# Kernel optimization log

Measured on AMD Instinct MI355X. Metric: run time of the kernel, lower is better.

## Reference

```python
import jax, jax.numpy as jnp
import numpy as np

N = 512
NODE_IN = 64
NODE_OUT = 64
ED_IN = 32
ED_OUT = 32
STATE = 80  # must satisfy 2*NODE_IN + ED_IN == 2*STATE
SLOPE = 0.1
EPS = 1e-5


def setup_inputs() -> dict:
    key = jax.random.key(0)
    ks = jax.random.split(key, 10)
    def lin(k, out_f, in_f):
        return jax.random.normal(k, (out_f, in_f), jnp.float32) / np.sqrt(in_f).astype(np.float32)
    x = jax.random.normal(ks[0], (N, NODE_IN), jnp.float32)
    edge_attr = jax.random.normal(ks[1], (N * N, ED_IN), jnp.float32)
    mask = jax.random.randint(ks[2], (N * N, 1), 0, 2).astype(jnp.int32)
    return {
        "x": x,
        "edge_attr": edge_attr,
        "mask": mask,
        "W_nu": lin(ks[3], NODE_OUT, NODE_IN),
        "b_nu": jnp.zeros((NODE_OUT,), jnp.float32),
        "W_h2": lin(ks[4], STATE, 2 * STATE),
        "b_h2": jnp.zeros((STATE,), jnp.float32),
        "W_eo": lin(ks[5], ED_OUT, STATE),
        "b_eo": jnp.zeros((ED_OUT,), jnp.float32),
        "e_vec": jax.random.normal(ks[6], (2 * NODE_OUT + ED_OUT,), jnp.float32) * 0.1,
        "bn_n_w": jnp.ones((NODE_OUT,), jnp.float32),
        "bn_n_b": jnp.zeros((NODE_OUT,), jnp.float32),
        "bn_e_w": jnp.ones((ED_OUT,), jnp.float32),
        "bn_e_b": jnp.zeros((ED_OUT,), jnp.float32),
    }


def _lrelu(v):
    return jax.nn.leaky_relu(v, SLOPE)


def _bn(v, w, b):
    # BatchNorm1d, training-mode (batch stats, biased variance)
    mu = v.mean(axis=0)
    var = v.var(axis=0)
    return (v - mu) / jnp.sqrt(var + EPS) * w + b


def reference(x, edge_attr, mask, W_nu, b_nu, W_h2, b_h2, W_eo, b_eo, e_vec,
              bn_n_w, bn_n_b, bn_e_w, bn_e_b):
    n = x.shape[0]
    m = mask.astype(x.dtype)  # [N*N, 1]
    # triplet_e[i*N+j] = [x_i, edge_attr_{ij}, x_j]
    src = jnp.repeat(x, n, axis=0)          # [N*N, NODE_IN]
    dst = jnp.tile(x, (n, 1))               # [N*N, NODE_IN]
    triplet_e = jnp.concatenate([src, edge_attr, dst], axis=-1)  # [N*N, 2*STATE]
    # NOTE: ed_trans_layer / ed_hidden_1 outputs are dead code in the source.
    h = _lrelu(triplet_e @ W_h2.T + b_h2)                 # [N*N, STATE]
    new_edge_attr = _lrelu(h @ W_eo.T + b_eo)             # [N*N, ED_OUT]
    new_edge_attr = new_edge_attr * m
    xn = _lrelu(x @ W_nu.T + b_nu)                        # [N, NODE_OUT]
    triplet_n = jnp.concatenate(
        [jnp.repeat(xn, n, axis=0), new_edge_attr, jnp.tile(xn, (n, 1))], axis=-1
    ).reshape(n, n, 2 * NODE_OUT + ED_OUT)
    scores = _lrelu(jnp.einsum("ijd,d->ij", triplet_n, e_vec))  # [N, N]
    att = jax.nn.softmax(scores, axis=1)
    att = (att.reshape(n * n, 1) * m).reshape(n, n)
    # dropout disabled (deterministic / eval)
    new_x = att @ xn                                       # [N, NODE_OUT]
    new_x = _bn(new_x, bn_n_w, bn_n_b)
    new_edge_attr = _bn(new_edge_attr, bn_e_w, bn_e_b)
    return new_x, new_edge_attr
```

## Files before the change

### kernel.cpp

```cpp
#include <hip/hip_runtime.h>

#define SLOPE 0.1f
#define EPS 1e-5f

typedef __bf16 bf16x8 __attribute__((ext_vector_type(8)));
typedef unsigned short u16x8 __attribute__((ext_vector_type(8)));
typedef float f32x4 __attribute__((ext_vector_type(4)));
typedef unsigned u32x4 __attribute__((ext_vector_type(4)));

#define WS_ESC 0
#define WS_ESH 32
#define WS_A 64
#define WS_B 576
#define WS_XN 1088
#define WS_NEWX 33856
#define WS_P1B 66624
#define WS_SC 107584
#define WS_PART 369728
#define WSH_WB 804992
#define WSH_WB2 810112
#define WSH_WO 812672
#define WSH_XB 815744
#define WSH_NE 848512

__device__ __forceinline__ float lrelu(float v) { return v > 0.f ? v : SLOPE * v; }
__device__ __forceinline__ unsigned short f2bf(float f) {
  unsigned x = __float_as_uint(f);
  return (unsigned short)((x + 0x7fffu + ((x >> 16) & 1u)) >> 16);
}
__device__ __forceinline__ float bf2f(unsigned short u) {
  return __uint_as_float(((unsigned)u) << 16);
}

__global__ void __launch_bounds__(256) k1(const float* __restrict__ x,
                                          const float* __restrict__ W_nu,
                                          const float* __restrict__ b_nu,
                                          const float* __restrict__ W_h2,
                                          const float* __restrict__ b_h2,
                                          const float* __restrict__ W_eo,
                                          const float* __restrict__ ev,
                                          float* ws) {
  int blk = blockIdx.x;
  int tid = threadIdx.x;
  unsigned short* wsh = (unsigned short*)ws;
  if (blk < 128) {
    __shared__ float wlds[64 * 65];
#pragma unroll
    for (int it = 0; it < 16; it++) {
      int idx = it * 256 + tid;
      wlds[(idx >> 6) * 65 + (idx & 63)] = W_nu[idx];
    }
    int gid = blk * 256 + tid;
    wsh[WSH_XB + gid] = f2bf(x[gid]);
    if (gid < 64) ws[WS_PART + gid] = 0.f;
    if (gid < 5120) {
      int c = gid / 2560, r = gid - c * 2560;
      int t = r >> 9, l = (r >> 3) & 63, jj = r & 7;
      int n = t * 16 + (l & 15);
      int k = (l >> 4) * 8 + jj + c * 32;
      wsh[WSH_WB + gid] = f2bf(W_h2[n * 160 + 64 + k]);
    } else if (gid < 7680) {
      int idx = gid - 5120;
      int t = idx >> 9, l = (idx >> 3) & 63, jj = idx & 7;
      int n = t * 16 + (l & 15);
      int k = (l >> 4) * 8 + jj;
      wsh[WSH_WB2 + idx] = f2bf(W_h2[n * 160 + 128 + k]);
    } else if (gid < 10752) {
      int idx = gid - 7680;
      int t2 = idx / 1536, r2 = idx - t2 * 1536;
      int s = r2 >> 9, l = (r2 >> 3) & 63, jj = r2 & 7;
      int n = t2 * 16 + (l & 15);
      int k = s * 32 + (l >> 4) * 8 + jj;
      wsh[WSH_WO + idx] = (k < 80) ? f2bf(W_eo[n * 80 + k]) : (unsigned short)0;
    }
    __syncthreads();
    int i = blk * 4 + (tid >> 6);
    int c = tid & 63;
    float acc = b_nu[c];
    const float* xr = x + i * 64;
#pragma unroll 8
    for (int k = 0; k < 64; k++) acc += xr[k] * wlds[c * 65 + k];
    float xnv = lrelu(acc);
    ws[WS_XN + i * 64 + c] = xnv;
    float va = xnv * ev[c];
    float vb = xnv * ev[96 + c];
#pragma unroll
    for (int off = 32; off >= 1; off >>= 1) {
      va += __shfl_xor(va, off, 64);
      vb += __shfl_xor(vb, off, 64);
    }
    if (c == 0) { ws[WS_A + i] = va; ws[WS_B + i] = vb; }
  } else {
    int b2 = blk - 128;
    int bm = b2 & 7, bn = b2 >> 3;
    int wave = tid >> 6, lane = tid & 63;
    int c16 = lane & 15, q = lane >> 4;
    int n = bn * 16 + c16;
    const float* wrow = W_h2 + n * 160;
    int mrow = bm * 64 + wave * 16 + c16;
    bf16x8 bfr[2], afr[2];
#pragma unroll
    for (int ks = 0; ks < 2; ks++) {
      const float* bs = wrow + ks * 32 + q * 8;
      const float* as = x + mrow * 64 + ks * 32 + q * 8;
      u16x8 ub, ua;
#pragma unroll
      for (int jj = 0; jj < 8; jj++) { ub[jj] = f2bf(bs[jj]); ua[jj] = f2bf(as[jj]); }
      bfr[ks] = __builtin_bit_cast(bf16x8, ub);
      afr[ks] = __builtin_bit_cast(bf16x8, ua);
    }
    float bias = b_h2[n];
    f32x4 acc = {bias, bias, bias, bias};
    acc = __builtin_amdgcn_mfma_f32_16x16x32_bf16(afr[0], bfr[0], acc, 0, 0, 0);
    acc = __builtin_amdgcn_mfma_f32_16x16x32_bf16(afr[1], bfr[1], acc, 0, 0, 0);
#pragma unroll
    for (int r = 0; r < 4; r++) {
      int mm = bm * 64 + wave * 16 + q * 4 + r;
      ws[WS_P1B + mm * 80 + n] = acc[r];
    }
  }
}

__global__ void __launch_bounds__(512) k2(const float* __restrict__ ea,
                                          const int* __restrict__ mask,
                                          const float* __restrict__ b_eo,
                                          const float* __restrict__ ev,
                                          float* ws) {
  __shared__ unsigned short wlds[10752];
  __shared__ unsigned short ht[128 * 104];
  __shared__ float p1s[80];
  __shared__ float s_row[512];
  __shared__ float red[8];
  __shared__ float nx[8][64];
  __shared__ float wred[2][8][32];
  int tid = threadIdx.x;
  int w = tid >> 6, lane = tid & 63;
  int c16 = lane & 15, q = lane >> 4;
  int i = blockIdx.x;
  const unsigned short* wsh = (const unsigned short*)ws;
  unsigned* ne32 = (unsigned*)((unsigned short*)ws + WSH_NE);

#pragma unroll
  for (int it = 0; it < 3; it++) {
    int idx = it * 512 + tid;
    if (idx < 1344) *(u16x8*)&wlds[idx * 8] = *(const u16x8*)(wsh + WSH_WB + idx * 8);
  }
  if (tid < 80) p1s[tid] = ws[WS_P1B + i * 80 + tid];
  float beo0 = b_eo[c16], beo1 = b_eo[16 + c16];
  float eve0 = ev[64 + c16], eve1 = ev[80 + c16];
  float a_i = ws[WS_A + i];
  __syncthreads();

  float scs0 = 0.f, scss0 = 0.f, scs1 = 0.f, scss1 = 0.f;

#pragma unroll
  for (int h = 0; h < 4; h++) {
    int jb = w * 64 + h * 16;

    bf16x8 af0;
    {
      const float* src = ea + (i * 512 + jb + c16) * 32 + q * 8;
      f32x4 e0 = *(const f32x4*)src;
      f32x4 e1 = *(const f32x4*)(src + 4);
      u16x8 u;
#pragma unroll
      for (int jj = 0; jj < 4; jj++) { u[jj] = f2bf(e0[jj]); u[4 + jj] = f2bf(e1[jj]); }
      af0 = __builtin_bit_cast(bf16x8, u);
    }
    bf16x8 af1 = __builtin_bit_cast(
        bf16x8, *(const u16x8*)(wsh + WSH_XB + (jb + c16) * 64 + q * 8));
    bf16x8 af2 = __builtin_bit_cast(
        bf16x8, *(const u16x8*)(wsh + WSH_XB + (jb + c16) * 64 + 32 + q * 8));
    int4 mk = *(const int4*)(mask + i * 512 + jb + q * 4);
    int mkv[4];
    mkv[0] = mk.x; mkv[1] = mk.y; mkv[2] = mk.z; mkv[3] = mk.w;

    f32x4 acc[5];
#pragma unroll
    for (int t = 0; t < 5; t++) {
      float p1v = p1s[t * 16 + c16];
      acc[t] = {p1v, p1v, p1v, p1v};
    }
#pragma unroll
    for (int t = 0; t < 5; t++) {
      bf16x8 wb = __builtin_bit_cast(bf16x8, *(const u16x8*)&wlds[t * 512 + lane * 8]);
      acc[t] = __builtin_amdgcn_mfma_f32_16x16x32_bf16(af0, wb, acc[t], 0, 0, 0);
    }
#pragma unroll
    for (int t = 0; t < 5; t++) {
      bf16x8 wb =
          __builtin_bit_cast(bf16x8, *(const u16x8*)&wlds[2560 + t * 512 + lane * 8]);
      acc[t] = __builtin_amdgcn_mfma_f32_16x16x32_bf16(af1, wb, acc[t], 0, 0, 0);
    }
#pragma unroll
    for (int t = 0; t < 5; t++) {
      bf16x8 wb =
          __builtin_bit_cast(bf16x8, *(const u16x8*)&wlds[5120 + t * 512 + lane * 8]);
      acc[t] = __builtin_amdgcn_mfma_f32_16x16x32_bf16(af2, wb, acc[t], 0, 0, 0);
    }
#pragma unroll
    for (int t = 0; t < 5; t++)
#pragma unroll
      for (int r = 0; r < 4; r++)
        ht[(w * 16 + q * 4 + r) * 104 + t * 16 + c16] = f2bf(lrelu(acc[t][r]));

    f32x4 acc2[2] = {{0.f, 0.f, 0.f, 0.f}, {0.f, 0.f, 0.f, 0.f}};
    int hrow = w * 16 + c16;
#pragma unroll
    for (int s = 0; s < 3; s++) {
      int kk = s * 32 + q * 8;
      u16x8 hb = {0, 0, 0, 0, 0, 0, 0, 0};
      if (kk < 80) hb = *(const u16x8*)&ht[hrow * 104 + kk];
      bf16x8 ha = __builtin_bit_cast(bf16x8, hb);
      bf16x8 wo0 =
          __builtin_bit_cast(bf16x8, *(const u16x8*)&wlds[7680 + s * 512 + lane * 8]);
      bf16x8 wo1 = __builtin_bit_cast(
          bf16x8, *(const u16x8*)&wlds[7680 + 1536 + s * 512 + lane * 8]);
      acc2[0] = __builtin_amdgcn_mfma_f32_16x16x32_bf16(ha, wo0, acc2[0], 0, 0, 0);
      acc2[1] = __builtin_amdgcn_mfma_f32_16x16x32_bf16(ha, wo1, acc2[1], 0, 0, 0);
    }

    float se[4];
#pragma unroll
    for (int r = 0; r < 4; r++) {
      int m = i * 512 + jb + q * 4 + r;
      float mf = mkv[r] ? 1.f : 0.f;
      float v0 = lrelu(acc2[0][r] + beo0) * mf;
      float v1 = lrelu(acc2[1][r] + beo1) * mf;
      scs0 += v0; scss0 += v0 * v0;
      scs1 += v1; scss1 += v1 * v1;
      ne32[m * 16 + c16] = (unsigned)f2bf(v0) | ((unsigned)f2bf(v1) << 16);
      float s = v0 * eve0 + v1 * eve1;
#pragma unroll
      for (int off = 8; off >= 1; off >>= 1) s += __shfl_xor(s, off, 64);
      se[r] = s;
    }
    if (c16 < 4) {
      int j = jb + q * 4 + c16;
      float s = (c16 == 0) ? se[0] : (c16 == 1) ? se[1] : (c16 == 2) ? se[2] : se[3];
      s_row[j] = lrelu(a_i + ws[WS_B + j] + s);
    }
  }

  scs0 += __shfl_xor(scs0, 16, 64); scs0 += __shfl_xor(scs0, 32, 64);
  scss0 += __shfl_xor(scss0, 16, 64); scss0 += __shfl_xor(scss0, 32, 64);
  scs1 += __shfl_xor(scs1, 16, 64); scs1 += __shfl_xor(scs1, 32, 64);
  scss1 += __shfl_xor(scss1, 16, 64); scss1 += __shfl_xor(scss1, 32, 64);
  if (q == 0) {
    wred[0][w][c16] = scs0; wred[0][w][16 + c16] = scs1;
    wred[1][w][c16] = scss0; wred[1][w][16 + c16] = scss1;
  }
  __syncthreads();

  float p = __expf(s_row[tid]);
  float sm = p;
#pragma unroll
  for (int off = 32; off >= 1; off >>= 1) sm += __shfl_xor(sm, off, 64);
  if (lane == 0) red[w] = sm;
  __syncthreads();
  float tot = red[0] + red[1] + red[2] + red[3] + red[4] + red[5] + red[6] + red[7];
  float attv = p * (1.f / tot) * (mask[i * 512 + tid] ? 1.f : 0.f);
  s_row[tid] = attv;
  __syncthreads();

  const float* xn = ws + WS_XN;
  float accv = 0.f;
#pragma unroll 4
  for (int u = 0; u < 64; u++) {
    int j = w * 64 + u;
    accv += s_row[j] * xn[j * 64 + lane];
  }
  nx[w][lane] = accv;
  __syncthreads();
  if (tid < 64) {
    float s = 0.f;
#pragma unroll
    for (int w2 = 0; w2 < 8; w2++) s += nx[w2][tid];
    ws[WS_NEWX + i * 64 + tid] = s;
    int half = tid >> 5, col = tid & 31;
    float v = 0.f;
#pragma unroll
    for (int w2 = 0; w2 < 8; w2++) v += wred[half][w2][col];
    atomicAdd(&ws[WS_PART + tid], v);
  }
}

__global__ void __launch_bounds__(256) k5(const float* __restrict__ bn_n_w,
                                          const float* __restrict__ bn_n_b,
                                          const float* __restrict__ bn_e_w,
                                          const float* __restrict__ bn_e_b,
                                          const float* __restrict__ ws,
                                          float* __restrict__ out) {
  int blk = blockIdx.x, tid = threadIdx.x;
  if (blk < 8) {
    __shared__ float s1[4][64], s2[4][64], scl[64], sh[64];
    int c = tid & 63, g = tid >> 6;
    float a = 0.f, b = 0.f;
#pragma unroll 4
    for (int u = 0; u < 128; u++) {
      float v = ws[WS_NEWX + (g * 128 + u) * 64 + c];
      a += v;
      b += v * v;
    }
    s1[g][c] = a;
    s2[g][c] = b;
    __syncthreads();
    if (tid < 64) {
      float sum = s1[0][tid] + s1[1][tid] + s1[2][tid] + s1[3][tid];
      float ssq = s2[0][tid] + s2[1][tid] + s2[2][tid] + s2[3][tid];
      float mean = sum * (1.f / 512.f);
      float var = ssq * (1.f / 512.f) - mean * mean;
      float s = bn_n_w[tid] * rsqrtf(fmaxf(var, 0.f) + EPS);
      scl[tid] = s;
      sh[tid] = bn_n_b[tid] - mean * s;
    }
    __syncthreads();
#pragma unroll 4
    for (int u = 0; u < 16; u++) {
      int idx = blk * 4096 + u * 256 + tid;
      int c2 = idx & 63;
      out[idx] = ws[WS_NEWX + idx] * scl[c2] + sh[c2];
    }
  } else {
    __shared__ __attribute__((aligned(16))) float escsh[64];
    if (tid < 32) {
      float sum = ws[WS_PART + tid];
      float ssq = ws[WS_PART + 32 + tid];
      float mean = sum * (1.f / 262144.f);
      float var = ssq * (1.f / 262144.f) - mean * mean;
      float s = bn_e_w[tid] * rsqrtf(fmaxf(var, 0.f) + EPS);
      escsh[tid] = s;
      escsh[32 + tid] = bn_e_b[tid] - mean * s;
    }
    __syncthreads();
    const unsigned* ne32 = (const unsigned*)((const unsigned short*)ws + WSH_NE);
    int b4 = ((blk - 8) * 256 + tid) * 4;
    u32x4 raw = *(const u32x4*)(ne32 + b4);
    int e32 = (b4 >> 4) * 32;
    int cb = b4 & 15;
    f32x4 esc0 = *(const f32x4*)&escsh[cb];
    f32x4 esc1 = *(const f32x4*)&escsh[16 + cb];
    f32x4 esh0 = *(const f32x4*)&escsh[32 + cb];
    f32x4 esh1 = *(const f32x4*)&escsh[48 + cb];
    f32x4 lo, hi;
#pragma unroll
    for (int u = 0; u < 4; u++) {
      lo[u] = bf2f((unsigned short)(raw[u] & 0xffffu)) * esc0[u] + esh0[u];
      hi[u] = bf2f((unsigned short)(raw[u] >> 16)) * esc1[u] + esh1[u];
    }
    float* oe = out + 32768;
    *(f32x4*)(oe + e32 + cb) = lo;
    *(f32x4*)(oe + e32 + 16 + cb) = hi;
  }
}

extern "C" void kernel_launch(void* const* d_in, const int* in_sizes, int n_in,
                              void* d_out, int out_size, void* d_ws, size_t ws_size,
                              hipStream_t stream) {
  const float* x = (const float*)d_in[0];
  const float* ea = (const float*)d_in[1];
  const int* mask = (const int*)d_in[2];
  const float* Wnu = (const float*)d_in[3];
  const float* bnu = (const float*)d_in[4];
  const float* Wh2 = (const float*)d_in[5];
  const float* bh2 = (const float*)d_in[6];
  const float* Weo = (const float*)d_in[7];
  const float* beo = (const float*)d_in[8];
  const float* ev = (const float*)d_in[9];
  const float* bnw = (const float*)d_in[10];
  const float* bnb = (const float*)d_in[11];
  const float* bew = (const float*)d_in[12];
  const float* beb = (const float*)d_in[13];
  float* ws = (float*)d_ws;
  float* out = (float*)d_out;

  k1<<<168, 256, 0, stream>>>(x, Wnu, bnu, Wh2, bh2, Weo, ev, ws);
  k2<<<512, 512, 0, stream>>>(ea, mask, beo, ev, ws);
  k5<<<4104, 256, 0, stream>>>(bnw, bnb, bew, beb, ws, out);
}
```

Before: 151.6 us.

## Fuse three kernels into one cooperative persistent kernel with grid syncs

```diff
diff --git a/kernel.cpp b/kernel.cpp
--- a/kernel.cpp
+++ b/kernel.cpp
@@ -1,4 +1,7 @@
 #include <hip/hip_runtime.h>
+#include <hip/hip_cooperative_groups.h>
+
+namespace cg = cooperative_groups;
 
 #define SLOPE 0.1f
 #define EPS 1e-5f
@@ -30,6 +33,347 @@
 }
 __device__ __forceinline__ float bf2f(unsigned short u) {
   return __uint_as_float(((unsigned)u) << 16);
+}
+
+__global__ void __launch_bounds__(512) kall(
+    const float* __restrict__ x, const float* __restrict__ ea,
+    const int* __restrict__ mask, const float* __restrict__ W_nu,
+    const float* __restrict__ b_nu, const float* __restrict__ W_h2,
+    const float* __restrict__ b_h2, const float* __restrict__ W_eo,
+    const float* __restrict__ b_eo, const float* __restrict__ ev,
+    const float* __restrict__ bn_n_w, const float* __restrict__ bn_n_b,
+    const float* __restrict__ bn_e_w, const float* __restrict__ bn_e_b,
+    float* ws, float* __restrict__ out) {
+  cg::grid_group gg = cg::this_grid();
+  __shared__ union __attribute__((aligned(16))) {
+    float wnu[64 * 65];
+    struct {
+      unsigned short wlds[10752];
+      unsigned short ht[128 * 104];
+      float p1s[80];
+      float s_row[512];
+      float red[8];
+      float nx[8][64];
+      float wred[2][8][32];
+    } p2;
+    struct {
+      float s1[8][64];
+      float s2[8][64];
+      float scl[64];
+      float shf[64];
+      float escsh[64];
+    } p3;
+  } sh;
+
+  int tid = threadIdx.x, blk = blockIdx.x;
+  int G = gridDim.x;
+  int gtid = blk * 512 + tid, gstride = G * 512;
+  unsigned short* wsh = (unsigned short*)ws;
+
+  for (int idx = gtid; idx < 32768; idx += gstride) wsh[WSH_XB + idx] = f2bf(x[idx]);
+  for (int idx = gtid; idx < 10752; idx += gstride) {
+    if (idx < 5120) {
+      int c = idx / 2560, r = idx - c * 2560;
+      int t = r >> 9, l = (r >> 3) & 63, jj = r & 7;
+      int n = t * 16 + (l & 15);
+      int k = (l >> 4) * 8 + jj + c * 32;
+      wsh[WSH_WB + idx] = f2bf(W_h2[n * 160 + 64 + k]);
+    } else if (idx < 7680) {
+      int i2 = idx - 5120;
+      int t = i2 >> 9, l = (i2 >> 3) & 63, jj = i2 & 7;
+      int n = t * 16 + (l & 15);
+      int k = (l >> 4) * 8 + jj;
+      wsh[WSH_WB2 + i2] = f2bf(W_h2[n * 160 + 128 + k]);
+    } else {
+      int i3 = idx - 7680;
+      int t2 = i3 / 1536, r2 = i3 - t2 * 1536;
+      int s = r2 >> 9, l = (r2 >> 3) & 63, jj = r2 & 7;
+      int n = t2 * 16 + (l & 15);
+      int k = s * 32 + (l >> 4) * 8 + jj;
+      wsh[WSH_WO + i3] = (k < 80) ? f2bf(W_eo[n * 80 + k]) : (unsigned short)0;
+    }
+  }
+  if (gtid < 64) ws[WS_PART + gtid] = 0.f;
+
+  {
+#pragma unroll
+    for (int it = 0; it < 8; it++) {
+      int idx = it * 512 + tid;
+      sh.wnu[(idx >> 6) * 65 + (idx & 63)] = W_nu[idx];
+    }
+    __syncthreads();
+    int c = tid & 63;
+    for (int r0 = blk * 8; r0 < 512; r0 += G * 8) {
+      int i = r0 + (tid >> 6);
+      float acc = b_nu[c];
+      const float* xr = x + i * 64;
+#pragma unroll 8
+      for (int k = 0; k < 64; k++) acc += xr[k] * sh.wnu[c * 65 + k];
+      float xnv = lrelu(acc);
+      ws[WS_XN + i * 64 + c] = xnv;
+      float va = xnv * ev[c];
+      float vb = xnv * ev[96 + c];
+#pragma unroll
+      for (int off = 32; off >= 1; off >>= 1) {
+        va += __shfl_xor(va, off, 64);
+        vb += __shfl_xor(vb, off, 64);
+      }
+      if (c == 0) { ws[WS_A + i] = va; ws[WS_B + i] = vb; }
+    }
+  }
+
+  {
+    int stid = tid & 255;
+    int wave = stid >> 6, lane = stid & 63;
+    int c16 = lane & 15, q = lane >> 4;
+    for (int u = blk * 2 + (tid >> 8); u < 40; u += G * 2) {
+      int bm = u & 7, bn = u >> 3;
+      int n = bn * 16 + c16;
+      const float* wrow = W_h2 + n * 160;
+      int mrow = bm * 64 + wave * 16 + c16;
+      bf16x8 bfr[2], afr[2];
+#pragma unroll
+      for (int ks = 0; ks < 2; ks++) {
+        const float* bs = wrow + ks * 32 + q * 8;
+        const float* as = x + mrow * 64 + ks * 32 + q * 8;
+        u16x8 ub, ua;
+#pragma unroll
+        for (int jj = 0; jj < 8; jj++) { ub[jj] = f2bf(bs[jj]); ua[jj] = f2bf(as[jj]); }
+        bfr[ks] = __builtin_bit_cast(bf16x8, ub);
+        afr[ks] = __builtin_bit_cast(bf16x8, ua);
+      }
+      float bias = b_h2[n];
+      f32x4 acc = {bias, bias, bias, bias};
+      acc = __builtin_amdgcn_mfma_f32_16x16x32_bf16(afr[0], bfr[0], acc, 0, 0, 0);
+      acc = __builtin_amdgcn_mfma_f32_16x16x32_bf16(afr[1], bfr[1], acc, 0, 0, 0);
+#pragma unroll
+      for (int r = 0; r < 4; r++) {
+        int mm = bm * 64 + wave * 16 + q * 4 + r;
+        ws[WS_P1B + mm * 80 + n] = acc[r];
+      }
+    }
+  }
+
+  gg.sync();
+
+  {
+    int w = tid >> 6, lane = tid & 63;
+    int c16 = lane & 15, q = lane >> 4;
+    unsigned* ne32 = (unsigned*)(wsh + WSH_NE);
+#pragma unroll
+    for (int it = 0; it < 3; it++) {
+      int idx = it * 512 + tid;
+      if (idx < 1344)
+        *(u16x8*)&sh.p2.wlds[idx * 8] = *(const u16x8*)(wsh + WSH_WB + idx * 8);
+    }
+    float beo0 = b_eo[c16], beo1 = b_eo[16 + c16];
+    float eve0 = ev[64 + c16], eve1 = ev[80 + c16];
+
+    for (int i = blk; i < 512; i += G) {
+      if (tid < 80) sh.p2.p1s[tid] = ws[WS_P1B + i * 80 + tid];
+      float a_i = ws[WS_A + i];
+      __syncthreads();
+
+      float scs0 = 0.f, scss0 = 0.f, scs1 = 0.f, scss1 = 0.f;
+#pragma unroll
+      for (int h = 0; h < 4; h++) {
+        int jb = w * 64 + h * 16;
+        bf16x8 af0;
+        {
+          const float* src = ea + (i * 512 + jb + c16) * 32 + q * 8;
+          f32x4 e0 = *(const f32x4*)src;
+          f32x4 e1 = *(const f32x4*)(src + 4);
+          u16x8 u;
+#pragma unroll
+          for (int jj = 0; jj < 4; jj++) { u[jj] = f2bf(e0[jj]); u[4 + jj] = f2bf(e1[jj]); }
+          af0 = __builtin_bit_cast(bf16x8, u);
+        }
+        bf16x8 af1 = __builtin_bit_cast(
+            bf16x8, *(const u16x8*)(wsh + WSH_XB + (jb + c16) * 64 + q * 8));
+        bf16x8 af2 = __builtin_bit_cast(
+            bf16x8, *(const u16x8*)(wsh + WSH_XB + (jb + c16) * 64 + 32 + q * 8));
+        int4 mk = *(const int4*)(mask + i * 512 + jb + q * 4);
+        int mkv[4];
+        mkv[0] = mk.x; mkv[1] = mk.y; mkv[2] = mk.z; mkv[3] = mk.w;
+
+        f32x4 acc[5];
+#pragma unroll
+        for (int t = 0; t < 5; t++) {
+          float p1v = sh.p2.p1s[t * 16 + c16];
+          acc[t] = {p1v, p1v, p1v, p1v};
+        }
+#pragma unroll
+        for (int t = 0; t < 5; t++) {
+          bf16x8 wb =
+              __builtin_bit_cast(bf16x8, *(const u16x8*)&sh.p2.wlds[t * 512 + lane * 8]);
+          acc[t] = __builtin_amdgcn_mfma_f32_16x16x32_bf16(af0, wb, acc[t], 0, 0, 0);
+        }
+#pragma unroll
+        for (int t = 0; t < 5; t++) {
+          bf16x8 wb = __builtin_bit_cast(
+              bf16x8, *(const u16x8*)&sh.p2.wlds[2560 + t * 512 + lane * 8]);
+          acc[t] = __builtin_amdgcn_mfma_f32_16x16x32_bf16(af1, wb, acc[t], 0, 0, 0);
+        }
+#pragma unroll
+        for (int t = 0; t < 5; t++) {
+          bf16x8 wb = __builtin_bit_cast(
+              bf16x8, *(const u16x8*)&sh.p2.wlds[5120 + t * 512 + lane * 8]);
+          acc[t] = __builtin_amdgcn_mfma_f32_16x16x32_bf16(af2, wb, acc[t], 0, 0, 0);
+        }
+#pragma unroll
+        for (int t = 0; t < 5; t++)
+#pragma unroll
+          for (int r = 0; r < 4; r++)
+            sh.p2.ht[(w * 16 + q * 4 + r) * 104 + t * 16 + c16] = f2bf(lrelu(acc[t][r]));
+
+        f32x4 acc2[2] = {{0.f, 0.f, 0.f, 0.f}, {0.f, 0.f, 0.f, 0.f}};
+        int hrow = w * 16 + c16;
+#pragma unroll
+        for (int s = 0; s < 3; s++) {
+          int kk = s * 32 + q * 8;
+          u16x8 hb = {0, 0, 0, 0, 0, 0, 0, 0};
+          if (kk < 80) hb = *(const u16x8*)&sh.p2.ht[hrow * 104 + kk];
+          bf16x8 ha = __builtin_bit_cast(bf16x8, hb);
+          bf16x8 wo0 = __builtin_bit_cast(
+              bf16x8, *(const u16x8*)&sh.p2.wlds[7680 + s * 512 + lane * 8]);
+          bf16x8 wo1 = __builtin_bit_cast(
+              bf16x8, *(const u16x8*)&sh.p2.wlds[7680 + 1536 + s * 512 + lane * 8]);
+          acc2[0] = __builtin_amdgcn_mfma_f32_16x16x32_bf16(ha, wo0, acc2[0], 0, 0, 0);
+          acc2[1] = __builtin_amdgcn_mfma_f32_16x16x32_bf16(ha, wo1, acc2[1], 0, 0, 0);
+        }
+
+        float se[4];
+#pragma unroll
+        for (int r = 0; r < 4; r++) {
+          int m = i * 512 + jb + q * 4 + r;
+          float mf = mkv[r] ? 1.f : 0.f;
+          float v0 = lrelu(acc2[0][r] + beo0) * mf;
+          float v1 = lrelu(acc2[1][r] + beo1) * mf;
+          scs0 += v0; scss0 += v0 * v0;
+          scs1 += v1; scss1 += v1 * v1;
+          ne32[m * 16 + c16] = (unsigned)f2bf(v0) | ((unsigned)f2bf(v1) << 16);
+          float s = v0 * eve0 + v1 * eve1;
+#pragma unroll
+          for (int off = 8; off >= 1; off >>= 1) s += __shfl_xor(s, off, 64);
+          se[r] = s;
+        }
+        if (c16 < 4) {
+          int j = jb + q * 4 + c16;
+          float s = (c16 == 0) ? se[0] : (c16 == 1) ? se[1] : (c16 == 2) ? se[2] : se[3];
+          sh.p2.s_row[j] = lrelu(a_i + ws[WS_B + j] + s);
+        }
+      }
+
+      scs0 += __shfl_xor(scs0, 16, 64); scs0 += __shfl_xor(scs0, 32, 64);
+      scss0 += __shfl_xor(scss0, 16, 64); scss0 += __shfl_xor(scss0, 32, 64);
+      scs1 += __shfl_xor(scs1, 16, 64); scs1 += __shfl_xor(scs1, 32, 64);
+      scss1 += __shfl_xor(scss1, 16, 64); scss1 += __shfl_xor(scss1, 32, 64);
+      if (q == 0) {
+        sh.p2.wred[0][w][c16] = scs0; sh.p2.wred[0][w][16 + c16] = scs1;
+        sh.p2.wred[1][w][c16] = scss0; sh.p2.wred[1][w][16 + c16] = scss1;
+      }
+      __syncthreads();
+
+      float p = __expf(sh.p2.s_row[tid]);
+      float sm = p;
+#pragma unroll
+      for (int off = 32; off >= 1; off >>= 1) sm += __shfl_xor(sm, off, 64);
+      if (lane == 0) sh.p2.red[w] = sm;
+      __syncthreads();
+      float tot = sh.p2.red[0] + sh.p2.red[1] + sh.p2.red[2] + sh.p2.red[3] +
+                  sh.p2.red[4] + sh.p2.red[5] + sh.p2.red[6] + sh.p2.red[7];
+      float attv = p * (1.f / tot) * (mask[i * 512 + tid] ? 1.f : 0.f);
+      __syncthreads();
+      sh.p2.s_row[tid] = attv;
+      __syncthreads();
+
+      const float* xn = ws + WS_XN;
+      float accv = 0.f;
+#pragma unroll 4
+      for (int u = 0; u < 64; u++) {
+        int j = w * 64 + u;
+        accv += sh.p2.s_row[j] * xn[j * 64 + lane];
+      }
+      sh.p2.nx[w][lane] = accv;
+      __syncthreads();
+      if (tid < 64) {
+        float s = 0.f;
+#pragma unroll
+        for (int w2 = 0; w2 < 8; w2++) s += sh.p2.nx[w2][tid];
+        ws[WS_NEWX + i * 64 + tid] = s;
+        int half = tid >> 5, col = tid & 31;
+        float v = 0.f;
+#pragma unroll
+        for (int w2 = 0; w2 < 8; w2++) v += sh.p2.wred[half][w2][col];
+        atomicAdd(&ws[WS_PART + tid], v);
+      }
+    }
+  }
+
+  gg.sync();
+
+  {
+    if (tid < 32) {
+      float sum = ws[WS_PART + tid];
+      float ssq = ws[WS_PART + 32 + tid];
+      float mean = sum * (1.f / 262144.f);
+      float var = ssq * (1.f / 262144.f) - mean * mean;
+      float s = bn_e_w[tid] * rsqrtf(fmaxf(var, 0.f) + EPS);
+      sh.p3.escsh[tid] = s;
+      sh.p3.escsh[32 + tid] = bn_e_b[tid] - mean * s;
+    }
+    if (blk < 8) {
+      int c = tid & 63, g = tid >> 6;
+      float a = 0.f, b = 0.f;
+#pragma unroll 4
+      for (int u = 0; u < 64; u++) {
+        float v = ws[WS_NEWX + (g * 64 + u) * 64 + c];
+        a += v;
+        b += v * v;
+      }
+      sh.p3.s1[g][c] = a;
+      sh.p3.s2[g][c] = b;
+      __syncthreads();
+      if (tid < 64) {
+        float sum = 0.f, ssq = 0.f;
+#pragma unroll
+        for (int g2 = 0; g2 < 8; g2++) { sum += sh.p3.s1[g2][tid]; ssq += sh.p3.s2[g2][tid]; }
+        float mean = sum * (1.f / 512.f);
+        float var = ssq * (1.f / 512.f) - mean * mean;
+        float s = bn_n_w[tid] * rsqrtf(fmaxf(var, 0.f) + EPS);
+        sh.p3.scl[tid] = s;
+        sh.p3.shf[tid] = bn_n_b[tid] - mean * s;
+      }
+      __syncthreads();
+#pragma unroll
+      for (int u = 0; u < 8; u++) {
+        int idx = blk * 4096 + u * 512 + tid;
+        int c2 = idx & 63;
+        out[idx] = ws[WS_NEWX + idx] * sh.p3.scl[c2] + sh.p3.shf[c2];
+      }
+    }
+    __syncthreads();
+    const unsigned* ne32c = (const unsigned*)(wsh + WSH_NE);
+    int cb = (tid & 3) << 2;
+    f32x4 esc0 = *(const f32x4*)&sh.p3.escsh[cb];
+    f32x4 esc1 = *(const f32x4*)&sh.p3.escsh[16 + cb];
+    f32x4 esh0 = *(const f32x4*)&sh.p3.escsh[32 + cb];
+    f32x4 esh1 = *(const f32x4*)&sh.p3.escsh[48 + cb];
+    float* oe = out + 32768;
+    for (int it2 = gtid; it2 < 1048576; it2 += gstride) {
+      int b4 = it2 * 4;
+      u32x4 raw = *(const u32x4*)(ne32c + b4);
+      int e32 = (b4 >> 4) * 32;
+      f32x4 lo, hi;
+#pragma unroll
+      for (int u = 0; u < 4; u++) {
+        lo[u] = bf2f((unsigned short)(raw[u] & 0xffffu)) * esc0[u] + esh0[u];
+        hi[u] = bf2f((unsigned short)(raw[u] >> 16)) * esc1[u] + esh1[u];
+      }
+      *(f32x4*)(oe + e32 + cb) = lo;
+      *(f32x4*)(oe + e32 + 16 + cb) = hi;
+    }
+  }
 }
 
 __global__ void __launch_bounds__(256) k1(const float* __restrict__ x,
@@ -139,7 +483,6 @@
   int i = blockIdx.x;
   const unsigned short* wsh = (const unsigned short*)ws;
   unsigned* ne32 = (unsigned*)((unsigned short*)ws + WSH_NE);
-
 #pragma unroll
   for (int it = 0; it < 3; it++) {
     int idx = it * 512 + tid;
@@ -150,13 +493,10 @@
   float eve0 = ev[64 + c16], eve1 = ev[80 + c16];
   float a_i = ws[WS_A + i];
   __syncthreads();
-
   float scs0 = 0.f, scss0 = 0.f, scs1 = 0.f, scss1 = 0.f;
-
 #pragma unroll
   for (int h = 0; h < 4; h++) {
     int jb = w * 64 + h * 16;
-
     bf16x8 af0;
     {
       const float* src = ea + (i * 512 + jb + c16) * 32 + q * 8;
@@ -174,7 +514,6 @@
     int4 mk = *(const int4*)(mask + i * 512 + jb + q * 4);
     int mkv[4];
     mkv[0] = mk.x; mkv[1] = mk.y; mkv[2] = mk.z; mkv[3] = mk.w;
-
     f32x4 acc[5];
 #pragma unroll
     for (int t = 0; t < 5; t++) {
@@ -203,7 +542,6 @@
 #pragma unroll
       for (int r = 0; r < 4; r++)
         ht[(w * 16 + q * 4 + r) * 104 + t * 16 + c16] = f2bf(lrelu(acc[t][r]));
-
     f32x4 acc2[2] = {{0.f, 0.f, 0.f, 0.f}, {0.f, 0.f, 0.f, 0.f}};
     int hrow = w * 16 + c16;
 #pragma unroll
@@ -219,7 +557,6 @@
       acc2[0] = __builtin_amdgcn_mfma_f32_16x16x32_bf16(ha, wo0, acc2[0], 0, 0, 0);
       acc2[1] = __builtin_amdgcn_mfma_f32_16x16x32_bf16(ha, wo1, acc2[1], 0, 0, 0);
     }
-
     float se[4];
 #pragma unroll
     for (int r = 0; r < 4; r++) {
@@ -241,7 +578,6 @@
       s_row[j] = lrelu(a_i + ws[WS_B + j] + s);
     }
   }
-
   scs0 += __shfl_xor(scs0, 16, 64); scs0 += __shfl_xor(scs0, 32, 64);
   scss0 += __shfl_xor(scss0, 16, 64); scss0 += __shfl_xor(scss0, 32, 64);
   scs1 += __shfl_xor(scs1, 16, 64); scs1 += __shfl_xor(scs1, 32, 64);
@@ -251,7 +587,6 @@
     wred[1][w][c16] = scss0; wred[1][w][16 + c16] = scss1;
   }
   __syncthreads();
-
   float p = __expf(s_row[tid]);
   float sm = p;
 #pragma unroll
@@ -262,7 +597,6 @@
   float attv = p * (1.f / tot) * (mask[i * 512 + tid] ? 1.f : 0.f);
   s_row[tid] = attv;
   __syncthreads();
-
   const float* xn = ws + WS_XN;
   float accv = 0.f;
 #pragma unroll 4
@@ -293,7 +627,7 @@
                                           float* __restrict__ out) {
   int blk = blockIdx.x, tid = threadIdx.x;
   if (blk < 8) {
-    __shared__ float s1[4][64], s2[4][64], scl[64], sh[64];
+    __shared__ float s1[4][64], s2[4][64], scl[64], shf[64];
     int c = tid & 63, g = tid >> 6;
     float a = 0.f, b = 0.f;
 #pragma unroll 4
@@ -312,14 +646,14 @@
       float var = ssq * (1.f / 512.f) - mean * mean;
       float s = bn_n_w[tid] * rsqrtf(fmaxf(var, 0.f) + EPS);
       scl[tid] = s;
-      sh[tid] = bn_n_b[tid] - mean * s;
+      shf[tid] = bn_n_b[tid] - mean * s;
     }
     __syncthreads();
 #pragma unroll 4
     for (int u = 0; u < 16; u++) {
       int idx = blk * 4096 + u * 256 + tid;
       int c2 = idx & 63;
-      out[idx] = ws[WS_NEWX + idx] * scl[c2] + sh[c2];
+      out[idx] = ws[WS_NEWX + idx] * scl[c2] + shf[c2];
     }
   } else {
     __shared__ __attribute__((aligned(16))) float escsh[64];
@@ -374,6 +708,34 @@
   float* ws = (float*)d_ws;
   float* out = (float*)d_out;
 
+  static int coop_state = -1;
+  static int gblocks = 0;
+  if (gblocks == 0) {
+    int per = 0;
+    if (hipOccupancyMaxActiveBlocksPerMultiprocessor(&per, kall, 512, 0) != hipSuccess ||
+        per < 1)
+      per = 1;
+    int cus = 256;
+    hipDeviceGetAttribute(&cus, hipDeviceAttributeMultiprocessorCount, 0);
+    long g = (long)per * (long)cus;
+    gblocks = (int)(g > 512 ? 512 : g);
+    if (gblocks < 8) gblocks = 8;
+  }
+
+  if (coop_state != 0) {
+    void* args[] = {(void*)&x,   (void*)&ea,  (void*)&mask, (void*)&Wnu,
+                    (void*)&bnu, (void*)&Wh2, (void*)&bh2,  (void*)&Weo,
+                    (void*)&beo, (void*)&ev,  (void*)&bnw,  (void*)&bnb,
+                    (void*)&bew, (void*)&beb, (void*)&ws,   (void*)&out};
+    hipError_t rc = hipLaunchCooperativeKernel(kall, dim3(gblocks), dim3(512), args,
+                                               0, stream);
+    if (rc == hipSuccess) {
+      coop_state = 1;
+      return;
+    }
+    coop_state = 0;
+  }
+
   k1<<<168, 256, 0, stream>>>(x, Wnu, bnu, Wh2, bh2, Weo, ev, ws);
   k2<<<512, 512, 0, stream>>>(ea, mask, beo, ev, ws);
   k5<<<4104, 256, 0, stream>>>(bnw, bnb, bew, beb, ws, out);
```

New measurement: 228.2 us. 50.6% more time.
